# Optimization experiments

Hardware: AMD Instinct MI355X
Metric: run time of the kernel (lower is better)

The kernel has to match this reference:

```python
import jax, jax.numpy as jnp
import numpy as np

NUM_HEADS = 16
THETA = 10000.0


def _rope(x, cos, sin):
    # x: [B, H, S, d_k]; cos/sin: [S, d_k//2] broadcast over B, H
    x1 = x[..., 0::2]
    x2 = x[..., 1::2]
    r1 = cos * x1 - sin * x2
    r2 = sin * x1 + cos * x2
    # interleave back: (..., half_d, 2) -> (..., d_k)
    return jnp.stack((r1, r2), axis=-1).reshape(x.shape)


def setup_inputs() -> dict:
    key = jax.random.key(0)
    ks = jax.random.split(key, 5)
    B, S, D = 4, 2048, 1024
    scale = D ** -0.5
    x = jax.random.normal(ks[0], (B, S, D), dtype=jnp.float32)
    wq = jax.random.normal(ks[1], (D, D), dtype=jnp.float32) * scale
    wk = jax.random.normal(ks[2], (D, D), dtype=jnp.float32) * scale
    wv = jax.random.normal(ks[3], (D, D), dtype=jnp.float32) * scale
    wo = jax.random.normal(ks[4], (D, D), dtype=jnp.float32) * scale
    return {"x": x, "wq": wq, "wk": wk, "wv": wv, "wo": wo}


def reference(x, wq, wk, wv, wo):
    B, S, D = x.shape
    H = NUM_HEADS
    dk = D // H

    def proj(w):
        # x @ w.T, split heads -> [B, H, S, dk]
        y = jnp.einsum('bsd,ed->bse', x, w)
        return y.reshape(B, S, H, dk).transpose(0, 2, 1, 3)

    q, k, v = proj(wq), proj(wk), proj(wv)

    # RoPE (interleaved pairs), positions = arange(S)
    inv_freq = THETA ** (-(jnp.arange(0, dk, 2, dtype=jnp.float32) / dk))
    ang = jnp.arange(S, dtype=jnp.float32)[:, None] * inv_freq  # [S, dk//2]
    cos, sin = jnp.cos(ang), jnp.sin(ang)
    q = _rope(q, cos, sin)
    k = _rope(k, cos, sin)

    scores = jnp.einsum('bhqd,bhkd->bhqk', q, k) / jnp.sqrt(jnp.asarray(dk, x.dtype))
    causal = jnp.tril(jnp.ones((S, S), dtype=bool))  # keep self + past
    scores = jnp.where(causal, scores, -jnp.inf)
    p = jax.nn.softmax(scores, axis=-1)
    attn = jnp.einsum('bhqk,bhkd->bhqd', p, v)
    attn = attn.transpose(0, 2, 1, 3).reshape(B, S, D)
    return jnp.einsum('bsd,ed->bse', attn, wo)
```

## Files before the change

kernel.cpp:

```cpp
#include <hip/hip_runtime.h>
#include <hip/hip_bf16.h>
#include <cstdint>
#include <cstddef>

#define Bb 4
#define Ss 2048
#define Dd 1024
#define Hh 16
#define Mm (Bb*Ss)

typedef __bf16 bf16_t;
typedef __bf16 bf16x8 __attribute__((ext_vector_type(8)));
typedef __bf16 bf16x4 __attribute__((ext_vector_type(4)));
typedef float  f32x4  __attribute__((ext_vector_type(4)));
typedef float  f32x16 __attribute__((ext_vector_type(16)));
typedef unsigned int u32x4 __attribute__((ext_vector_type(4)));
typedef unsigned int u32x2 __attribute__((ext_vector_type(2)));

#define MFMA16(a,b,c) __builtin_amdgcn_mfma_f32_16x16x32_bf16(a,b,c,0,0,0)
#define MFMA32(a,b,c) __builtin_amdgcn_mfma_f32_32x32x16_bf16(a,b,c,0,0,0)

#define QSCALE 0.18033688011112042f

static __device__ __forceinline__ float fexp2(float x) {
#if __has_builtin(__builtin_amdgcn_exp2f)
  return __builtin_amdgcn_exp2f(x);
#else
  return exp2f(x);
#endif
}

static __device__ __forceinline__ bf16x8 ld16g(const bf16_t* p) {
  return __builtin_bit_cast(bf16x8, *reinterpret_cast<const u32x4*>(p));
}

static __device__ __forceinline__ void gload_lds16(const bf16_t* g, bf16_t* l) {
  __builtin_amdgcn_global_load_lds(
      (__attribute__((address_space(1))) void*)(g),
      (__attribute__((address_space(3))) void*)(l),
      16, 0, 0);
}

__global__ void cvt_f32_bf16(const float* __restrict__ in, bf16_t* __restrict__ out) {
  int i = (blockIdx.x * blockDim.x + threadIdx.x) * 4;
  float4 f = *reinterpret_cast<const float4*>(in + i);
  out[i + 0] = (bf16_t)f.x;
  out[i + 1] = (bf16_t)f.y;
  out[i + 2] = (bf16_t)f.z;
  out[i + 3] = (bf16_t)f.w;
}

__global__ void cvt_w4(const float* __restrict__ w0, const float* __restrict__ w1,
                       const float* __restrict__ w2, const float* __restrict__ w3,
                       bf16_t* __restrict__ out) {
  int bid = blockIdx.x;
  int seg = bid >> 10, local = bid & 1023;
  const float* w = (seg == 0) ? w0 : (seg == 1) ? w1 : (seg == 2) ? w2 : w3;
  int i = (local * 256 + threadIdx.x) * 4;
  float4 f = *reinterpret_cast<const float4*>(w + i);
  bf16_t* o = out + (size_t)seg * (Dd * Dd) + i;
  o[0] = (bf16_t)f.x; o[1] = (bf16_t)f.y; o[2] = (bf16_t)f.z; o[3] = (bf16_t)f.w;
}

__global__ void rope_tab_k(float2* __restrict__ tab) {
  int idx = blockIdx.x * 256 + threadIdx.x;
  int i = idx & 31, s = idx >> 5;
  float inv_freq = exp2f(-(float)i * (13.2877123795494f / 32.0f));
  float ang = (float)s * inv_freq;
  float sn, cs;
  sincosf(ang, &sn, &cs);
  tab[idx] = make_float2(cs, sn);
}

template <typename OutT>
__global__ __launch_bounds__(256, 2) void gemm3(const bf16_t* __restrict__ A,
                                                const bf16_t* __restrict__ Bm,
                                                OutT* __restrict__ C0,
                                                OutT* __restrict__ C1,
                                                OutT* __restrict__ C2,
                                                const float2* __restrict__ tab,
                                                int Kdim) {
  __shared__ bf16_t As[3][256 * 32];
  __shared__ bf16_t Bs[3][128 * 32];
  const int t = threadIdx.x;
  const int lane = t & 63, w = t >> 6;
  const int l15 = lane & 15, lg = lane >> 4;
  const int wr = w >> 1, wc = w & 1;
  const int m0 = blockIdx.x * 256, n0 = blockIdx.y * 128;

  const bf16_t* gA[4];
#pragma unroll
  for (int i = 0; i < 4; ++i) {
    int q = i * 256 + t, row = q >> 2, sl = (q & 3) ^ ((row >> 1) & 3);
    gA[i] = A + (size_t)(m0 + row) * Kdim + sl * 8;
  }
  const bf16_t* gB[2];
#pragma unroll
  for (int i = 0; i < 2; ++i) {
    int q = i * 256 + t, row = q >> 2, sl = (q & 3) ^ ((row >> 1) & 3);
    gB[i] = Bm + (size_t)(n0 + row) * Kdim + sl * 8;
  }
  const int wb = w * 64 * 8;

  auto stage = [&](int slot, int kb0) {
#pragma unroll
    for (int i = 0; i < 4; ++i)
      gload_lds16(gA[i] + kb0, &As[slot][i * 2048 + wb]);
#pragma unroll
    for (int i = 0; i < 2; ++i)
      gload_lds16(gB[i] + kb0, &Bs[slot][i * 2048 + wb]);
  };

  int aoff[8], boff[4];
#pragma unroll
  for (int i = 0; i < 8; ++i) {
    int row = wr * 128 + i * 16 + l15;
    aoff[i] = row * 32 + ((lg ^ ((row >> 1) & 3)) * 8);
  }
#pragma unroll
  for (int j = 0; j < 4; ++j) {
    int row = wc * 64 + j * 16 + l15;
    boff[j] = row * 32 + ((lg ^ ((row >> 1) & 3)) * 8);
  }

  f32x4 acc[8][4] = {};
  const int KT = Kdim / 32;

  stage(0, 0);
  stage(1, 32);
  for (int j = 0; j < KT; ++j) {
    if (j == KT - 1) {
      asm volatile("s_waitcnt vmcnt(0) lgkmcnt(0)" ::: "memory");
    } else {
      asm volatile("s_waitcnt vmcnt(6) lgkmcnt(0)" ::: "memory");
    }
    __builtin_amdgcn_s_barrier();
    if (j + 2 < KT) stage((j + 2) % 3, (j + 2) * 32);
    const bf16_t* ab = As[j % 3];
    const bf16_t* bb = Bs[j % 3];
    bf16x8 a[8], b[4];
#pragma unroll
    for (int jj = 0; jj < 4; ++jj)
      b[jj] = __builtin_bit_cast(bf16x8,
               *reinterpret_cast<const u32x4*>(bb + boff[jj]));
#pragma unroll
    for (int i = 0; i < 8; ++i)
      a[i] = __builtin_bit_cast(bf16x8,
               *reinterpret_cast<const u32x4*>(ab + aoff[i]));
    __builtin_amdgcn_s_setprio(1);
#pragma unroll
    for (int i = 0; i < 8; ++i)
#pragma unroll
      for (int jj = 0; jj < 4; ++jj)
        acc[i][jj] = MFMA16(a[i], b[jj], acc[i][jj]);
    __builtin_amdgcn_s_setprio(0);
  }

  OutT* Cs = (n0 < 1024) ? C0 : (n0 < 2048 ? C1 : C2);
  const int nb = n0 & 1023;
  const bool doRope = (tab != nullptr) && (n0 < 2048);
  const float qs = (n0 < 1024) ? QSCALE : 1.0f;

  if (doRope) {
#pragma unroll
    for (int i = 0; i < 8; ++i) {
      int rowb = m0 + wr * 128 + i * 16 + lg * 4;
#pragma unroll
      for (int j = 0; j < 4; ++j) {
        int col = nb + wc * 64 + j * 16 + l15;
        int i0 = (col & 63) >> 1;
        const bool ev = !(col & 1);
#pragma unroll
        for (int r = 0; r < 4; ++r) {
          float v = acc[i][j][r];
          float px = __shfl_xor(v, 1);
          int s = (rowb + r) & (Ss - 1);
          float2 f = tab[s * 32 + i0];
          float sn = ev ? -f.y : f.y;
          Cs[(size_t)(rowb + r) * 1024 + col] = (OutT)((f.x * v + sn * px) * qs);
        }
      }
    }
  } else {
#pragma unroll
    for (int i = 0; i < 8; ++i) {
      int rowb = m0 + wr * 128 + i * 16 + lg * 4;
#pragma unroll
      for (int j = 0; j < 4; ++j) {
        int col = nb + wc * 64 + j * 16 + l15;
#pragma unroll
        for (int r = 0; r < 4; ++r)
          Cs[(size_t)(rowb + r) * 1024 + col] = (OutT)acc[i][j][r];
      }
    }
  }
}

__global__ __launch_bounds__(256) void transpose_v(const bf16_t* __restrict__ V,
                                                   bf16_t* __restrict__ Vt) {
  __shared__ bf16_t tile[64][72];
  int bh = blockIdx.y;
  int b = bh >> 4, h = bh & 15;
  int s0 = blockIdx.x * 64;
  int t = threadIdx.x;
  const bf16_t* vbase = V + (size_t)b * Ss * Dd + h * 64;
#pragma unroll
  for (int c = 0; c < 2; ++c) {
    int cf = c * 256 + t;
    int s = cf >> 3, d8 = cf & 7;
    u32x4 v = *reinterpret_cast<const u32x4*>(vbase + (size_t)(s0 + s) * Dd + d8 * 8);
    *reinterpret_cast<u32x4*>(&tile[s][d8 * 8]) = v;
  }
  __syncthreads();
  bf16_t* obase = Vt + (size_t)bh * 64 * Ss;
#pragma unroll
  for (int c = 0; c < 2; ++c) {
    int cf = c * 256 + t;
    int d = cf >> 3, s8 = cf & 7;
    __align__(16) bf16_t tmp[8];
#pragma unroll
    for (int i = 0; i < 8; ++i) tmp[i] = tile[s8 * 8 + i][d];
    *reinterpret_cast<u32x4*>(obase + (size_t)d * Ss + s0 + s8 * 8) =
        *reinterpret_cast<const u32x4*>(tmp);
  }
}

__global__ __launch_bounds__(256, 2) void attn_k(const bf16_t* __restrict__ Q,
                                                 const bf16_t* __restrict__ K,
                                                 const bf16_t* __restrict__ Vt,
                                                 bf16_t* __restrict__ O) {
  __shared__ bf16_t Ks[3][4096];
  __shared__ bf16_t Vs[3][4096];
  const int t = threadIdx.x, lane = t & 63, w = t >> 6;
  const int l31 = lane & 31, hi = lane >> 5, hi8 = hi * 8;
  const int bh = blockIdx.y, b = bh >> 4, h = bh & 15;
  const int bx = blockIdx.x;
  const int i = bx * 4 + w;
  const int q0a = 32 * i, q0b = 2016 - 32 * i;
  const int dtA = q0a >> 6, hfA = (q0a >> 5) & 1;
  const int dtB = q0b >> 6, hfB = (q0b >> 5) & 1;
  const int NT = 32 - 2 * bx;
  const bf16_t* qb = Q + (size_t)b * Ss * Dd + h * 64;
  const bf16_t* kb = K + (size_t)b * Ss * Dd + h * 64;
  const bf16_t* vtb = Vt + (size_t)bh * 64 * Ss;

  const int a_ = l31 >> 2, c_ = l31 & 3;
  const int tau = (a_ >> 1) + 2 * (a_ & 1) + ((a_ & 4) >> 1);
  const int sig = c_ + 4 * tau;

  int kfoff[4];
#pragma unroll
  for (int c = 0; c < 4; ++c) {
    int j = sig >> 1, u = (sig & 1) * 8 + c * 2 + hi;
    kfoff[c] = j * 128 + ((u ^ j) * 8);
  }
  int vfoff[2][2];
#pragma unroll
  for (int db = 0; db < 2; ++db)
#pragma unroll
    for (int ks = 0; ks < 2; ++ks) {
      int d = db * 32 + l31, j = d >> 2, u = (d & 3) * 4 + ks * 2 + hi;
      vfoff[db][ks] = j * 128 + ((u ^ j) * 8);
    }

  const int sj = t >> 4, ss = t & 15, su = ss ^ sj;
  const bf16_t* ksrc0 = kb + (size_t)(2 * sj + (su >> 3)) * Dd + (su & 7) * 8;
  const bf16_t* vsrc0 = vtb + (size_t)(4 * sj + (su >> 2)) * Ss + (su & 3) * 8;

  auto stage = [&](int buf, int kb0) {
    bf16_t* kd = &Ks[buf][w * 512];
    bf16_t* vd = &Vs[buf][w * 512];
    gload_lds16(ksrc0 + (size_t)kb0 * Dd, kd);
    gload_lds16(ksrc0 + (size_t)(kb0 + 32) * Dd, kd + 2048);
    gload_lds16(vsrc0 + kb0, vd);
    gload_lds16(vsrc0 + kb0 + 32, vd + 2048);
  };

  bf16x8 qf[2][4];
#pragma unroll
  for (int c = 0; c < 4; ++c) {
    qf[0][c] = ld16g(qb + (size_t)(q0a + l31) * Dd + c * 16 + hi8);
    qf[1][c] = ld16g(qb + (size_t)(q0b + l31) * Dd + c * 16 + hi8);
  }

  float l_[2] = {0.f, 0.f};
  f32x16 o_[2][2] = {};

  auto chain = [&](int kt, int dt, int hf, bf16x8 (&qc)[4],
                   f32x16& o0, f32x16& o1, float& lc,
                   bf16x8 (&kf)[2][4], bf16x8 (&vf)[2][2][2]) {
    if (kt > dt) return;
    const bool last = (kt == dt);
    const bool do1 = !(last && hf == 0);
    f32x16 s0 = {}, s1 = {};
    __builtin_amdgcn_s_setprio(1);
    s0 = MFMA32(kf[0][0], qc[0], s0);
    s0 = MFMA32(kf[0][1], qc[1], s0);
    s0 = MFMA32(kf[0][2], qc[2], s0);
    s0 = MFMA32(kf[0][3], qc[3], s0);
    if (do1) {
      s1 = MFMA32(kf[1][0], qc[0], s1);
      s1 = MFMA32(kf[1][1], qc[1], s1);
      s1 = MFMA32(kf[1][2], qc[2], s1);
      s1 = MFMA32(kf[1][3], qc[3], s1);
    }
    __builtin_amdgcn_s_setprio(0);
    if (last) {
      if (hf) {
#pragma unroll
        for (int reg = 0; reg < 16; ++reg) {
          const int koff = (reg & 3) + 4 * (reg >> 2) + 8 * ((reg >> 2) >> 1) + hi8;
          s1[reg] = (koff <= l31) ? s1[reg] : -INFINITY;
        }
      } else {
#pragma unroll
        for (int reg = 0; reg < 16; ++reg) {
          const int koff = (reg & 3) + 4 * (reg >> 2) + 8 * ((reg >> 2) >> 1) + hi8;
          s0[reg] = (koff <= l31) ? s0[reg] : -INFINITY;
        }
      }
    }
    float p0[16], p1[16];
#pragma unroll
    for (int r = 0; r < 16; ++r) p0[r] = fexp2(s0[r]);
    bf16x8 pa0, pa1, pb0, pb1;
#pragma unroll
    for (int r = 0; r < 8; ++r) { pa0[r] = (bf16_t)p0[r]; pa1[r] = (bf16_t)p0[r + 8]; }
    if (do1) {
#pragma unroll
      for (int r = 0; r < 16; ++r) p1[r] = fexp2(s1[r]);
#pragma unroll
      for (int r = 0; r < 8; ++r) { pb0[r] = (bf16_t)p1[r]; pb1[r] = (bf16_t)p1[r + 8]; }
#pragma unroll
      for (int r = 0; r < 16; ++r) p0[r] += p1[r];
    }
#pragma unroll
    for (int st2 = 8; st2 > 0; st2 >>= 1)
#pragma unroll
      for (int r = 0; r < st2; ++r) p0[r] += p0[r + st2];
    lc += p0[0];
    __builtin_amdgcn_s_setprio(1);
    o0 = MFMA32(vf[0][0][0], pa0, o0);
    o0 = MFMA32(vf[0][0][1], pa1, o0);
    o1 = MFMA32(vf[0][1][0], pa0, o1);
    o1 = MFMA32(vf[0][1][1], pa1, o1);
    if (do1) {
      o0 = MFMA32(vf[1][0][0], pb0, o0);
      o0 = MFMA32(vf[1][0][1], pb1, o0);
      o1 = MFMA32(vf[1][1][0], pb0, o1);
      o1 = MFMA32(vf[1][1][1], pb1, o1);
    }
    __builtin_amdgcn_s_setprio(0);
  };

  stage(0, 0);
  stage(1, 64);
  for (int j = 0; j < NT; ++j) {
    if (j == NT - 1) {
      asm volatile("s_waitcnt vmcnt(0) lgkmcnt(0)" ::: "memory");
    } else {
      asm volatile("s_waitcnt vmcnt(4) lgkmcnt(0)" ::: "memory");
    }
    __builtin_amdgcn_s_barrier();
    if (j + 2 < NT) stage((j + 2) % 3, (j + 2) * 64);
    const bf16_t* kbuf = &Ks[j % 3][0];
    const bf16_t* vbuf = &Vs[j % 3][0];
    bf16x8 kf[2][4], vf[2][2][2];
#pragma unroll
    for (int st = 0; st < 2; ++st)
#pragma unroll
      for (int c = 0; c < 4; ++c)
        kf[st][c] = __builtin_bit_cast(bf16x8,
            *reinterpret_cast<const u32x4*>(kbuf + st * 2048 + kfoff[c]));
#pragma unroll
    for (int st = 0; st < 2; ++st)
#pragma unroll
      for (int db = 0; db < 2; ++db)
#pragma unroll
        for (int ks = 0; ks < 2; ++ks)
          vf[st][db][ks] = __builtin_bit_cast(bf16x8,
              *reinterpret_cast<const u32x4*>(vbuf + st * 2048 + vfoff[db][ks]));
    chain(j, dtA, hfA, qf[0], o_[0][0], o_[0][1], l_[0], kf, vf);
    chain(j, dtB, hfB, qf[1], o_[1][0], o_[1][1], l_[1], kf, vf);
  }

#pragma unroll
  for (int ch = 0; ch < 2; ++ch) {
    const float ltot = l_[ch] + __shfl_xor(l_[ch], 32);
    const float inv = 1.0f / ltot;
    const size_t rowoff = ((size_t)b * Ss + (ch ? q0b : q0a) + l31) * Dd + h * 64;
#pragma unroll
    for (int db = 0; db < 2; ++db)
#pragma unroll
      for (int tt = 0; tt < 4; ++tt) {
        bf16x4 ov;
#pragma unroll
        for (int c = 0; c < 4; ++c) ov[c] = (bf16_t)(o_[ch][db][4 * tt + c] * inv);
        *reinterpret_cast<u32x2*>(&O[rowoff + db * 32 + 8 * tt + 4 * hi]) =
            __builtin_bit_cast(u32x2, ov);
      }
  }
}

extern "C" void kernel_launch(void* const* d_in, const int* in_sizes, int n_in,
                              void* d_out, int out_size, void* d_ws, size_t ws_size,
                              hipStream_t stream) {
  (void)in_sizes; (void)n_in; (void)out_size; (void)ws_size;
  const float* x  = (const float*)d_in[0];
  const float* wq = (const float*)d_in[1];
  const float* wk = (const float*)d_in[2];
  const float* wv = (const float*)d_in[3];
  const float* wo = (const float*)d_in[4];
  float* out = (float*)d_out;

  char* ws = (char*)d_ws;
  const size_t MB16 = 16u << 20;
  bf16_t* xb   = (bf16_t*)(ws + 0);
  bf16_t* Qb   = (bf16_t*)(ws + 1 * MB16);
  bf16_t* Kb   = (bf16_t*)(ws + 2 * MB16);
  bf16_t* Vb   = (bf16_t*)(ws + 3 * MB16);
  bf16_t* wqkv = (bf16_t*)(ws + 4 * MB16);
  bf16_t* wob  = wqkv + 3u * Dd * Dd;
  float2* tab  = (float2*)(ws + 4 * MB16 + (8u << 20));
  bf16_t* Vt   = xb;
  bf16_t* AOb  = Vb;

  cvt_f32_bf16<<<(Mm * Dd) / 1024, 256, 0, stream>>>(x, xb);
  cvt_w4<<<4096, 256, 0, stream>>>(wq, wk, wv, wo, wqkv);
  rope_tab_k<<<256, 256, 0, stream>>>(tab);

  gemm3<bf16_t><<<dim3(Mm / 256, 24), 256, 0, stream>>>(xb, wqkv, Qb, Kb, Vb,
                                                        tab, Dd);

  transpose_v<<<dim3(Ss / 64, Bb * Hh), 256, 0, stream>>>(Vb, Vt);

  attn_k<<<dim3(8, Bb * Hh), 256, 0, stream>>>(Qb, Kb, Vt, AOb);

  gemm3<float><<<dim3(Mm / 256, 8), 256, 0, stream>>>(AOb, wob, out, out, out,
                                                      nullptr, Dd);
}
```

Measured before the change: 196.3 us.

## Use 256x256 tiles with 8 waves and interleaved staged loads in GEMM

The projection GEMM now uses 512-thread blocks covering 256x256 output tiles instead of 256x128, so each block reuses A across twice as many columns. Global-to-LDS staging for the next k-step is split into four parts, each interleaved with a quarter of the MFMA work and separated by barriers, to spread memory traffic over the compute. This doubles B's LDS footprint and adds extra barriers per k-iteration. It also halves the grid size, which may reduce occupancy, especially for the output GEMM, which now launches only 128 blocks.

```diff
diff --git a/kernel.cpp b/kernel.cpp
--- a/kernel.cpp
+++ b/kernel.cpp
@@ -73,86 +73,117 @@
 }
 
 template <typename OutT>
-__global__ __launch_bounds__(256, 2) void gemm3(const bf16_t* __restrict__ A,
-                                                const bf16_t* __restrict__ Bm,
-                                                OutT* __restrict__ C0,
-                                                OutT* __restrict__ C1,
-                                                OutT* __restrict__ C2,
-                                                const float2* __restrict__ tab,
-                                                int Kdim) {
+__global__ __launch_bounds__(512, 2) void gemm8p(const bf16_t* __restrict__ A,
+                                                 const bf16_t* __restrict__ Bm,
+                                                 OutT* __restrict__ C0,
+                                                 OutT* __restrict__ C1,
+                                                 OutT* __restrict__ C2,
+                                                 const float2* __restrict__ tab,
+                                                 int Kdim) {
   __shared__ bf16_t As[3][256 * 32];
-  __shared__ bf16_t Bs[3][128 * 32];
+  __shared__ bf16_t Bs[3][256 * 32];
   const int t = threadIdx.x;
   const int lane = t & 63, w = t >> 6;
   const int l15 = lane & 15, lg = lane >> 4;
-  const int wr = w >> 1, wc = w & 1;
-  const int m0 = blockIdx.x * 256, n0 = blockIdx.y * 128;
-
-  const bf16_t* gA[4];
-#pragma unroll
-  for (int i = 0; i < 4; ++i) {
-    int q = i * 256 + t, row = q >> 2, sl = (q & 3) ^ ((row >> 1) & 3);
-    gA[i] = A + (size_t)(m0 + row) * Kdim + sl * 8;
-  }
+  const int wm = w >> 2, wn = w & 3;
+  const int m0 = blockIdx.x * 256, n0 = blockIdx.y * 256;
+
+  const bf16_t* gA[2];
   const bf16_t* gB[2];
 #pragma unroll
   for (int i = 0; i < 2; ++i) {
-    int q = i * 256 + t, row = q >> 2, sl = (q & 3) ^ ((row >> 1) & 3);
+    int q = i * 512 + t, row = q >> 2, sl = (q & 3) ^ ((row >> 1) & 3);
+    gA[i] = A  + (size_t)(m0 + row) * Kdim + sl * 8;
     gB[i] = Bm + (size_t)(n0 + row) * Kdim + sl * 8;
   }
   const int wb = w * 64 * 8;
 
-  auto stage = [&](int slot, int kb0) {
-#pragma unroll
-    for (int i = 0; i < 4; ++i)
-      gload_lds16(gA[i] + kb0, &As[slot][i * 2048 + wb]);
-#pragma unroll
-    for (int i = 0; i < 2; ++i)
-      gload_lds16(gB[i] + kb0, &Bs[slot][i * 2048 + wb]);
+  auto stageP = [&](int slot, int k0, int part) {
+    if (part == 0)      gload_lds16(gA[0] + k0, &As[slot][wb]);
+    else if (part == 1) gload_lds16(gA[1] + k0, &As[slot][4096 + wb]);
+    else if (part == 2) gload_lds16(gB[0] + k0, &Bs[slot][wb]);
+    else                gload_lds16(gB[1] + k0, &Bs[slot][4096 + wb]);
   };
 
   int aoff[8], boff[4];
 #pragma unroll
   for (int i = 0; i < 8; ++i) {
-    int row = wr * 128 + i * 16 + l15;
+    int row = wm * 128 + i * 16 + l15;
     aoff[i] = row * 32 + ((lg ^ ((row >> 1) & 3)) * 8);
   }
 #pragma unroll
   for (int j = 0; j < 4; ++j) {
-    int row = wc * 64 + j * 16 + l15;
+    int row = wn * 64 + j * 16 + l15;
     boff[j] = row * 32 + ((lg ^ ((row >> 1) & 3)) * 8);
   }
 
   f32x4 acc[8][4] = {};
   const int KT = Kdim / 32;
 
-  stage(0, 0);
-  stage(1, 32);
+#pragma unroll
+  for (int p = 0; p < 4; ++p) stageP(0, 0, p);
+#pragma unroll
+  for (int p = 0; p < 4; ++p) stageP(1, 32, p);
+
   for (int j = 0; j < KT; ++j) {
     if (j == KT - 1) {
       asm volatile("s_waitcnt vmcnt(0) lgkmcnt(0)" ::: "memory");
     } else {
-      asm volatile("s_waitcnt vmcnt(6) lgkmcnt(0)" ::: "memory");
+      asm volatile("s_waitcnt vmcnt(4) lgkmcnt(0)" ::: "memory");
     }
     __builtin_amdgcn_s_barrier();
-    if (j + 2 < KT) stage((j + 2) % 3, (j + 2) * 32);
-    const bf16_t* ab = As[j % 3];
-    const bf16_t* bb = Bs[j % 3];
+    const int slot = j % 3, nslot = (j + 2) % 3, k2 = (j + 2) * 32;
+    const bool doStage = (j + 2 < KT);
+    const bf16_t* ab = As[slot];
+    const bf16_t* bb = Bs[slot];
     bf16x8 a[8], b[4];
+
 #pragma unroll
     for (int jj = 0; jj < 4; ++jj)
-      b[jj] = __builtin_bit_cast(bf16x8,
-               *reinterpret_cast<const u32x4*>(bb + boff[jj]));
-#pragma unroll
-    for (int i = 0; i < 8; ++i)
-      a[i] = __builtin_bit_cast(bf16x8,
-               *reinterpret_cast<const u32x4*>(ab + aoff[i]));
-    __builtin_amdgcn_s_setprio(1);
-#pragma unroll
-    for (int i = 0; i < 8; ++i)
-#pragma unroll
-      for (int jj = 0; jj < 4; ++jj)
-        acc[i][jj] = MFMA16(a[i], b[jj], acc[i][jj]);
+      b[jj] = __builtin_bit_cast(bf16x8, *reinterpret_cast<const u32x4*>(bb + boff[jj]));
+#pragma unroll
+    for (int i = 0; i < 4; ++i)
+      a[i] = __builtin_bit_cast(bf16x8, *reinterpret_cast<const u32x4*>(ab + aoff[i]));
+    if (doStage) stageP(nslot, k2, 0);
+    __builtin_amdgcn_s_setprio(1);
+#pragma unroll
+    for (int i = 0; i < 4; ++i) {
+      acc[i][0] = MFMA16(a[i], b[0], acc[i][0]);
+      acc[i][1] = MFMA16(a[i], b[1], acc[i][1]);
+    }
+    __builtin_amdgcn_s_setprio(0);
+    __builtin_amdgcn_s_barrier();
+
+    if (doStage) stageP(nslot, k2, 1);
+    __builtin_amdgcn_s_setprio(1);
+#pragma unroll
+    for (int i = 0; i < 4; ++i) {
+      acc[i][2] = MFMA16(a[i], b[2], acc[i][2]);
+      acc[i][3] = MFMA16(a[i], b[3], acc[i][3]);
+    }
+    __builtin_amdgcn_s_setprio(0);
+    __builtin_amdgcn_s_barrier();
+
+#pragma unroll
+    for (int i = 4; i < 8; ++i)
+      a[i] = __builtin_bit_cast(bf16x8, *reinterpret_cast<const u32x4*>(ab + aoff[i]));
+    if (doStage) stageP(nslot, k2, 2);
+    __builtin_amdgcn_s_setprio(1);
+#pragma unroll
+    for (int i = 4; i < 8; ++i) {
+      acc[i][0] = MFMA16(a[i], b[0], acc[i][0]);
+      acc[i][1] = MFMA16(a[i], b[1], acc[i][1]);
+    }
+    __builtin_amdgcn_s_setprio(0);
+    __builtin_amdgcn_s_barrier();
+
+    if (doStage) stageP(nslot, k2, 3);
+    __builtin_amdgcn_s_setprio(1);
+#pragma unroll
+    for (int i = 4; i < 8; ++i) {
+      acc[i][2] = MFMA16(a[i], b[2], acc[i][2]);
+      acc[i][3] = MFMA16(a[i], b[3], acc[i][3]);
+    }
     __builtin_amdgcn_s_setprio(0);
   }
 
@@ -164,10 +195,10 @@
   if (doRope) {
 #pragma unroll
     for (int i = 0; i < 8; ++i) {
-      int rowb = m0 + wr * 128 + i * 16 + lg * 4;
+      int rowb = m0 + wm * 128 + i * 16 + lg * 4;
 #pragma unroll
       for (int j = 0; j < 4; ++j) {
-        int col = nb + wc * 64 + j * 16 + l15;
+        int col = nb + wn * 64 + j * 16 + l15;
         int i0 = (col & 63) >> 1;
         const bool ev = !(col & 1);
 #pragma unroll
@@ -184,10 +215,10 @@
   } else {
 #pragma unroll
     for (int i = 0; i < 8; ++i) {
-      int rowb = m0 + wr * 128 + i * 16 + lg * 4;
+      int rowb = m0 + wm * 128 + i * 16 + lg * 4;
 #pragma unroll
       for (int j = 0; j < 4; ++j) {
-        int col = nb + wc * 64 + j * 16 + l15;
+        int col = nb + wn * 64 + j * 16 + l15;
 #pragma unroll
         for (int r = 0; r < 4; ++r)
           Cs[(size_t)(rowb + r) * 1024 + col] = (OutT)acc[i][j][r];
@@ -429,13 +460,13 @@
   cvt_w4<<<4096, 256, 0, stream>>>(wq, wk, wv, wo, wqkv);
   rope_tab_k<<<256, 256, 0, stream>>>(tab);
 
-  gemm3<bf16_t><<<dim3(Mm / 256, 24), 256, 0, stream>>>(xb, wqkv, Qb, Kb, Vb,
-                                                        tab, Dd);
+  gemm8p<bf16_t><<<dim3(Mm / 256, 12), 512, 0, stream>>>(xb, wqkv, Qb, Kb, Vb,
+                                                         tab, Dd);
 
   transpose_v<<<dim3(Ss / 64, Bb * Hh), 256, 0, stream>>>(Vb, Vt);
 
   attn_k<<<dim3(8, Bb * Hh), 256, 0, stream>>>(Qb, Kb, Vt, AOb);
 
-  gemm3<float><<<dim3(Mm / 256, 8), 256, 0, stream>>>(AOb, wob, out, out, out,
-                                                      nullptr, Dd);
-}
+  gemm8p<float><<<dim3(Mm / 256, 4), 512, 0, stream>>>(AOb, wob, out, out, out,
+                                                       nullptr, Dd);
+}
```

After: 198.9 us. No clear change (+1.3%).
